# Kernel tuning notes

Hardware: AMD Instinct MI355X
Metric: run time of the kernel (lower is better)

## Reference

```python
import jax, jax.numpy as jnp
import numpy as np

B, S, H, NH = 4, 2048, 1024, 16
HD = H // NH


def setup_inputs() -> dict:
    key = jax.random.key(0)
    ks = jax.random.split(key, 8)
    x = jax.random.normal(ks[0], (B, S, H), dtype=jnp.float32)
    y = jax.random.normal(ks[1], (B, S, H), dtype=jnp.float32)
    mask = jnp.zeros((B, S), dtype=bool)  # key padding mask; True = masked
    s = 0.02
    Wq_w = jax.random.normal(ks[2], (H, H), dtype=jnp.float32) * s
    Wq_b = jnp.zeros((H,), dtype=jnp.float32)
    Wkv_w = jax.random.normal(ks[3], (H, 2 * H), dtype=jnp.float32) * s
    Wkv_b = jnp.zeros((2 * H,), dtype=jnp.float32)
    Wo_w = jax.random.normal(ks[4], (H, H), dtype=jnp.float32) * s
    Wo_b = jnp.zeros((H,), dtype=jnp.float32)
    return {"x": x, "y": y, "mask": mask, "Wq_w": Wq_w, "Wq_b": Wq_b,
            "Wkv_w": Wkv_w, "Wkv_b": Wkv_b, "Wo_w": Wo_w, "Wo_b": Wo_b}


def reference(x, y, mask, Wq_w, Wq_b, Wkv_w, Wkv_b, Wo_w, Wo_b):
    b, s, c = x.shape
    # q: [B, NH, S, HD]
    q = (x @ Wq_w + Wq_b).reshape(b, s, NH, HD).transpose(0, 2, 1, 3)
    # kv: [B, S, 2, NH, HD] -> k, v: [B, NH, S, HD]
    kv = (y @ Wkv_w + Wkv_b).reshape(b, s, 2, NH, HD)
    k = kv[:, :, 0].transpose(0, 2, 1, 3)
    v = kv[:, :, 1].transpose(0, 2, 1, 3)
    attn = jnp.einsum("bhqd,bhkd->bhqk", q, k) / jnp.sqrt(jnp.float32(HD))
    causal = jnp.triu(jnp.ones((s, s), dtype=bool), k=1)  # True above diag = masked
    combined = causal[None, None, :, :] | mask[:, None, None, :]
    attn = jnp.where(combined, -jnp.inf, attn)
    attn = jax.nn.softmax(attn, axis=-1)
    # dropout is identity in eval mode
    out = jnp.einsum("bhqk,bhkd->bhqd", attn, v)
    out = out.transpose(0, 2, 1, 3).reshape(b, s, c)
    return out @ Wo_w + Wo_b
```

## Files before the change

### kernel.cpp

```cpp
#include <hip/hip_runtime.h>


#define Bv   4
#define Sv   2048
#define Hv   1024
#define NHv  16
#define HDv  64

typedef __attribute__((ext_vector_type(8))) short s16x8;
typedef __attribute__((ext_vector_type(4))) short s16x4;
typedef __attribute__((ext_vector_type(4))) float f32x4;

__device__ __forceinline__ short f2bf(float f) {
  unsigned u = __float_as_uint(f);
  unsigned r = (u + 0x7fffu + ((u >> 16) & 1u)) >> 16;
  return (short)r;
}

#if __has_builtin(__builtin_amdgcn_exp2f)
#define EXP2(x) __builtin_amdgcn_exp2f(x)
#else
#define EXP2(x) exp2f(x)
#endif

__device__ __forceinline__ void gl_lds16(const short* g, short* l) {
  __builtin_amdgcn_global_load_lds(
      (const __attribute__((address_space(1))) unsigned int*)g,
      (__attribute__((address_space(3))) unsigned int*)l, 16, 0, 0);
}

__global__ __launch_bounds__(256) void cvt2_bf16(const float* __restrict__ x,
                                                 const float* __restrict__ y,
                                                 short* __restrict__ Xb,
                                                 short* __restrict__ Yb, int nper) {
  int half = gridDim.x >> 1;
  int bid = blockIdx.x;
  const float* in = (bid < half) ? x : y;
  short* out = (bid < half) ? Xb : Yb;
  int lb = (bid < half) ? bid : bid - half;
  int i = (lb * 256 + threadIdx.x) * 4;
  if (i < nper) {
    float4 v = *(const float4*)&in[i];
    short r0 = f2bf(v.x), r1 = f2bf(v.y), r2 = f2bf(v.z), r3 = f2bf(v.w);
    unsigned long long pk = (unsigned long long)(unsigned short)r0
                          | ((unsigned long long)(unsigned short)r1 << 16)
                          | ((unsigned long long)(unsigned short)r2 << 32)
                          | ((unsigned long long)(unsigned short)r3 << 48);
    *(unsigned long long*)&out[i] = pk;
  }
}

__global__ __launch_bounds__(256)
void tcvt3(const float* __restrict__ Wq, const float* __restrict__ Wkv,
           const float* __restrict__ Wo, short* __restrict__ Wt,
           short* __restrict__ Wot) {
  __shared__ float tile[32][33];
  int bx = blockIdx.x;
  const float* in;
  short* out;
  int C, cx;
  if (bx < 32)       { in = Wq;  out = Wt;                          C = 1024; cx = bx; }
  else if (bx < 96)  { in = Wkv; out = Wt + (size_t)Hv * Hv;        C = 2048; cx = bx - 32; }
  else               { in = Wo;  out = Wot;                         C = 1024; cx = bx - 96; }
  const int R = 1024;
  int tx = threadIdx.x & 31, ty = threadIdx.x >> 5;
  int c0 = cx * 32, r0 = blockIdx.y * 32;
#pragma unroll
  for (int i = 0; i < 32; i += 8)
    tile[ty + i][tx] = in[(size_t)(r0 + ty + i) * C + c0 + tx];
  __syncthreads();
#pragma unroll
  for (int i = 0; i < 32; i += 8)
    out[(size_t)(c0 + ty + i) * R + r0 + tx] = f2bf(tile[tx][ty + i]);
}

__global__ __launch_bounds__(256)
void gemm_qkv(const short* __restrict__ Xb, const short* __restrict__ Yb,
              const short* __restrict__ Wt, const float* __restrict__ Wqb,
              const float* __restrict__ Wkvb, short* __restrict__ Qb,
              short* __restrict__ Kb, short* __restrict__ Vt) {
  __shared__ union SMem {
    struct { short A[2][128 * 64]; short B[2][128 * 64]; } g;
    short ep[128 * 136];
  } sm;
  const int tid = threadIdx.x;
  const int w = tid >> 6, l = tid & 63;
  const int wr = w >> 1, wc = w & 1;
  const int m0 = blockIdx.x * 128, n0 = blockIdx.y * 128;
  const short* A = (n0 < 1024) ? Xb : Yb;
  const int sel = n0 >> 10;

  auto STAGE = [&](int k0, int bi) {
#pragma unroll
    for (int i = 0; i < 4; ++i) {
      int c = tid + i * 256;
      int r = c >> 3;
      int u = (c & 7) ^ (r & 7);
      gl_lds16(&A[(size_t)(m0 + r) * Hv + k0 + u * 8], &sm.g.A[bi][c * 8]);
      gl_lds16(&Wt[(size_t)(n0 + r) * Hv + k0 + u * 8], &sm.g.B[bi][c * 8]);
    }
  };

  f32x4 acc[4][4] = {};

  auto KSTEP = [&](int kt) {
    const int buf = kt & 1;
#pragma unroll
    for (int kk = 0; kk < 64; kk += 32) {
      s16x8 af[4], bf[4];
#pragma unroll
      for (int m = 0; m < 4; ++m) {
        int row = wr * 64 + m * 16 + (l & 15);
        int sb = (row * 128 + kk * 2 + ((l >> 4) << 4)) ^ ((row & 7) << 4);
        af[m] = *(s16x8*)((char*)sm.g.A[buf] + sb);
      }
#pragma unroll
      for (int n = 0; n < 4; ++n) {
        int row = wc * 64 + n * 16 + (l & 15);
        int sb = (row * 128 + kk * 2 + ((l >> 4) << 4)) ^ ((row & 7) << 4);
        bf[n] = *(s16x8*)((char*)sm.g.B[buf] + sb);
      }
#pragma unroll
      for (int m = 0; m < 4; ++m)
#pragma unroll
        for (int n = 0; n < 4; ++n)
          acc[m][n] = __builtin_amdgcn_mfma_f32_16x16x32_bf16(af[m], bf[n], acc[m][n], 0, 0, 0);
    }
  };

  STAGE(0, 0);
  STAGE(64, 1);

  for (int kt = 0; kt < 15; ++kt) {
    asm volatile("s_waitcnt vmcnt(8)" ::: "memory");
    __builtin_amdgcn_s_barrier();
    __builtin_amdgcn_sched_barrier(0);
    KSTEP(kt);
    __builtin_amdgcn_s_barrier();
    __builtin_amdgcn_sched_barrier(0);
    if (kt + 2 < 16) STAGE((kt + 2) * 64, kt & 1);
  }
  asm volatile("s_waitcnt vmcnt(0)" ::: "memory");
  __builtin_amdgcn_s_barrier();
  __builtin_amdgcn_sched_barrier(0);
  KSTEP(15);
  __syncthreads();

  const int b = m0 >> 11, s0 = m0 & (Sv - 1);
  if (sel < 2) {
    const float scale = (sel == 0) ? 0.1803368801f : 1.0f;
    const float* bias = (sel == 0) ? Wqb : (Wkvb + (n0 - 1024));
#pragma unroll
    for (int m = 0; m < 4; ++m)
#pragma unroll
      for (int n = 0; n < 4; ++n) {
        int scol = wc * 64 + n * 16 + (l & 15);
#pragma unroll
        for (int e = 0; e < 4; ++e) {
          int srow = wr * 64 + m * 16 + ((l >> 4) << 2) + e;
          float v = (acc[m][n][e] + bias[scol]) * scale;
          sm.ep[srow * 136 + scol] = f2bf(v);
        }
      }
    __syncthreads();
    short* dst = sel ? Kb : Qb;
    const int hbase = (n0 & 1023) >> 6;
#pragma unroll
    for (int p = 0; p < 8; ++p) {
      int u = p * 256 + tid;
      int row = u >> 4, hf = (u >> 3) & 1, sub = u & 7;
      s16x8 vdat = *(s16x8*)&sm.ep[row * 136 + hf * 64 + sub * 8];
      *(s16x8*)&dst[(((size_t)(b * NHv + hbase + hf)) * Sv + s0 + row) * HDv + sub * 8] = vdat;
    }
  } else {
    const float* bias = Wkvb + (n0 - 1024);
#pragma unroll
    for (int m = 0; m < 4; ++m)
#pragma unroll
      for (int n = 0; n < 4; ++n) {
        int scol = wc * 64 + n * 16 + (l & 15);
        int srow0 = wr * 64 + m * 16 + ((l >> 4) << 2);
        s16x4 t;
#pragma unroll
        for (int e = 0; e < 4; ++e) t[e] = f2bf(acc[m][n][e] + bias[scol]);
        *(s16x4*)&sm.ep[scol * 136 + srow0] = t;
      }
    __syncthreads();
    const int hbase = (n0 - 2048) >> 6;
#pragma unroll
    for (int p = 0; p < 8; ++p) {
      int u = p * 256 + tid;
      int col = u >> 4, seg = u & 15;
      s16x8 vdat = *(s16x8*)&sm.ep[col * 136 + seg * 8];
      *(s16x8*)&Vt[(((size_t)(b * NHv + hbase + (col >> 6))) * HDv + (col & 63)) * Sv + s0 + seg * 8] = vdat;
    }
  }
}

__global__ __launch_bounds__(256)
void gemm_out(const short* __restrict__ A, const short* __restrict__ Bt,
              const float* __restrict__ bias, float* __restrict__ outf) {
  __shared__ short Alds[2][128 * 64];
  __shared__ short Blds[2][128 * 64];
  const int tid = threadIdx.x;
  const int w = tid >> 6, l = tid & 63;
  const int wr = w >> 1, wc = w & 1;
  const int m0 = blockIdx.x * 128, n0 = blockIdx.y * 128;

  auto STAGE = [&](int k0, int bi) {
#pragma unroll
    for (int i = 0; i < 4; ++i) {
      int c = tid + i * 256;
      int r = c >> 3;
      int u = (c & 7) ^ (r & 7);
      gl_lds16(&A[(size_t)(m0 + r) * Hv + k0 + u * 8], &Alds[bi][c * 8]);
      gl_lds16(&Bt[(size_t)(n0 + r) * Hv + k0 + u * 8], &Blds[bi][c * 8]);
    }
  };

  f32x4 acc[4][4] = {};

  STAGE(0, 0);
  __syncthreads();
  for (int kt = 0; kt < 16; ++kt) {
    const int buf = kt & 1;
    if (kt < 15) STAGE((kt + 1) * 64, buf ^ 1);
#pragma unroll
    for (int kk = 0; kk < 64; kk += 32) {
      s16x8 af[4], bf[4];
#pragma unroll
      for (int m = 0; m < 4; ++m) {
        int row = wr * 64 + m * 16 + (l & 15);
        int sb = (row * 128 + kk * 2 + ((l >> 4) << 4)) ^ ((row & 7) << 4);
        af[m] = *(s16x8*)((char*)Alds[buf] + sb);
      }
#pragma unroll
      for (int n = 0; n < 4; ++n) {
        int row = wc * 64 + n * 16 + (l & 15);
        int sb = (row * 128 + kk * 2 + ((l >> 4) << 4)) ^ ((row & 7) << 4);
        bf[n] = *(s16x8*)((char*)Blds[buf] + sb);
      }
#pragma unroll
      for (int m = 0; m < 4; ++m)
#pragma unroll
        for (int n = 0; n < 4; ++n)
          acc[m][n] = __builtin_amdgcn_mfma_f32_16x16x32_bf16(af[m], bf[n], acc[m][n], 0, 0, 0);
    }
    __syncthreads();
  }

#pragma unroll
  for (int m = 0; m < 4; ++m)
#pragma unroll
    for (int n = 0; n < 4; ++n)
#pragma unroll
      for (int e = 0; e < 4; ++e) {
        int gr = m0 + wr * 64 + m * 16 + ((l >> 4) << 2) + e;
        int gc = n0 + wc * 64 + n * 16 + (l & 15);
        outf[(size_t)gr * Hv + gc] = acc[m][n][e] + bias[gc];
      }
}

__global__ __launch_bounds__(512)
void attn_mfma(const short* __restrict__ Q, const short* __restrict__ Kb,
               const short* __restrict__ Vt, const unsigned char* __restrict__ msk,
               short* __restrict__ AO) {
  __shared__ short Klds[2][64 * 64];
  __shared__ short Vlds[2][64 * 64];
  __shared__ short Plds[8 * 32 * 64];
  __shared__ unsigned long long mword[2];

  const int tid = threadIdx.x;
  const int w = tid >> 6, l = tid & 63;
  const int il = l & 15, g = l >> 4;
  const int bh = blockIdx.x & 63;
  const int qb = 7 - (blockIdx.x >> 6);
  const int b = bh >> 4, h = bh & 15;
  const int q0 = qb * 256 + w * 32;

  int kvA0[4], pfA0[2];
#pragma unroll
  for (int n = 0; n < 4; ++n) {
    int row = n * 16 + il;
    kvA0[n] = row * 128 + ((g << 4) ^ ((row & 7) << 4));
  }
#pragma unroll
  for (int m = 0; m < 2; ++m) {
    int row = m * 16 + il;
    pfA0[m] = row * 128 + ((g << 4) ^ ((row & 7) << 4));
  }
  const int swzq = (il & 7) << 4;
  const int g8 = g << 3;

  s16x8 qf[2][2];
  const short* qbase = &Q[((size_t)bh * Sv + q0) * HDv];
#pragma unroll
  for (int m = 0; m < 2; ++m)
#pragma unroll
    for (int kk = 0; kk < 2; ++kk)
      qf[m][kk] = *(const s16x8*)&qbase[(m * 16 + il) * 64 + kk * 32 + (g << 3)];

  s16x8 onesf;
#pragma unroll
  for (int e2 = 0; e2 < 8; ++e2) onesf[e2] = (short)0x3F80;

  f32x4 oacc[2][4] = {};
  f32x4 lacc[2] = {};
  const f32x4 cinit = {-16.f, -16.f, -16.f, -16.f};

  char* const pbase = (char*)Plds + w * 4096;
  const short* kg0 = &Kb[(size_t)bh * Sv * HDv];
  const short* vg0 = &Vt[(size_t)bh * HDv * Sv];
  const int nkt = qb * 4 + 4;

  auto stageKV = [&](int t, int bufi) {
    const short* kg = kg0 + (size_t)t * 64 * HDv;
    const short* vg = vg0 + t * 64;
    int c = tid;
    int r = c >> 3;
    int u = (c & 7) ^ (r & 7);
    gl_lds16(&kg[(size_t)r * HDv + u * 8], &Klds[bufi][c * 8]);
    gl_lds16(&vg[(size_t)r * Sv + u * 8], &Vlds[bufi][c * 8]);
  };

  stageKV(0, 0);
  if (w == 0) {
    unsigned long long mwb = __ballot(msk[b * Sv + l] != 0);
    if (l == 0) mword[0] = mwb;
  }
  __syncthreads();

  for (int kt = 0; kt < nkt; ++kt) {
    const int k0 = kt * 64;
    const int buf = kt & 1;
    if (kt + 1 < nkt) {
      stageKV(kt + 1, buf ^ 1);
      if (w == 0) {
        unsigned long long mwb = __ballot(msk[b * Sv + (kt + 1) * 64 + l] != 0);
        if (l == 0) mword[buf ^ 1] = mwb;
      }
    }

    if (k0 <= q0 + 31) {
      const unsigned long long mw = mword[buf];
      const char* kldsb = (const char*)Klds[buf];
      const char* vldsb = (const char*)Vlds[buf];
      f32x4 sacc[4][2];
#pragma unroll
      for (int n = 0; n < 4; ++n)
#pragma unroll
        for (int m = 0; m < 2; ++m)
          sacc[n][m] = cinit;
      __builtin_amdgcn_s_setprio(1);
#pragma unroll
      for (int kk = 0; kk < 2; ++kk) {
        s16x8 kf[4];
#pragma unroll
        for (int n = 0; n < 4; ++n)
          kf[n] = *(s16x8*)(kldsb + (kvA0[n] ^ (kk << 6)));
#pragma unroll
        for (int n = 0; n < 4; ++n)
#pragma unroll
          for (int m = 0; m < 2; ++m)
            sacc[n][m] = __builtin_amdgcn_mfma_f32_16x16x32_bf16(kf[n], qf[m][kk], sacc[n][m], 0, 0, 0);
      }
      __builtin_amdgcn_s_setprio(0);

      if ((k0 + 63 > q0) || (mw != 0)) {
#pragma unroll
        for (int n = 0; n < 4; ++n)
#pragma unroll
          for (int m = 0; m < 2; ++m)
#pragma unroll
            for (int e = 0; e < 4; ++e) {
              int klocal = n * 16 + (g << 2) + e;
              int qg = q0 + m * 16 + il;
              bool bad = (k0 + klocal > qg) || ((mw >> klocal) & 1ull);
              if (bad) sacc[n][m][e] = -1e30f;
            }
      }

#pragma unroll
      for (int kk = 0; kk < 2; ++kk) {
#pragma unroll
        for (int m = 0; m < 2; ++m) {
          int pwb = (m * 16 + il) * 128;
#pragma unroll
          for (int n = kk * 2; n < kk * 2 + 2; ++n) {
            s16x4 t;
#pragma unroll
            for (int e = 0; e < 4; ++e) {
              float pv = EXP2(sacc[n][m][e]);
              t[e] = (short)(__float_as_uint(pv) >> 16);
            }
            *(s16x4*)(pbase + pwb + (((n << 5) + g8) ^ swzq)) = t;
          }
        }
        s16x8 pf[2], vf[4];
#pragma unroll
        for (int m = 0; m < 2; ++m)
          pf[m] = *(s16x8*)(pbase + (pfA0[m] ^ (kk << 6)));
#pragma unroll
        for (int n = 0; n < 4; ++n)
          vf[n] = *(s16x8*)(vldsb + (kvA0[n] ^ (kk << 6)));
        __builtin_amdgcn_s_setprio(1);
#pragma unroll
        for (int m = 0; m < 2; ++m) {
#pragma unroll
          for (int n = 0; n < 4; ++n)
            oacc[m][n] = __builtin_amdgcn_mfma_f32_16x16x32_bf16(pf[m], vf[n], oacc[m][n], 0, 0, 0);
          lacc[m] = __builtin_amdgcn_mfma_f32_16x16x32_bf16(pf[m], onesf, lacc[m], 0, 0, 0);
        }
        __builtin_amdgcn_s_setprio(0);
      }
    }
    __syncthreads();
  }

#pragma unroll
  for (int m = 0; m < 2; ++m)
#pragma unroll
    for (int e = 0; e < 4; ++e) {
      float inv = 1.f / lacc[m][e];
#pragma unroll
      for (int n = 0; n < 4; ++n) {
        int qg = q0 + m * 16 + (g << 2) + e;
        int dcol = n * 16 + il;
        AO[((size_t)b * Sv + qg) * Hv + h * HDv + dcol] = f2bf(oacc[m][n][e] * inv);
      }
    }
}

extern "C" void kernel_launch(void* const* d_in, const int* in_sizes, int n_in,
                              void* d_out, int out_size, void* d_ws, size_t ws_size,
                              hipStream_t stream) {
  (void)in_sizes; (void)n_in; (void)out_size; (void)ws_size;
  const float* x    = (const float*)d_in[0];
  const float* y    = (const float*)d_in[1];
  const unsigned char* msk = (const unsigned char*)d_in[2];
  const float* Wq   = (const float*)d_in[3];
  const float* Wqb  = (const float*)d_in[4];
  const float* Wkv  = (const float*)d_in[5];
  const float* Wkvb = (const float*)d_in[6];
  const float* Wo   = (const float*)d_in[7];
  const float* Wob  = (const float*)d_in[8];
  float* out = (float*)d_out;

  char* p = (char*)d_ws;
  auto alloc = [&](size_t bytes) {
    char* r = p;
    p += (bytes + 255) & ~(size_t)255;
    return r;
  };
  const size_t MT = (size_t)Bv * Sv;
  short* Xb   = (short*)alloc(MT * Hv * 2);
  short* Yb   = (short*)alloc(MT * Hv * 2);
  short* Wt   = (short*)alloc((size_t)3 * Hv * Hv * 2);
  short* Wot  = (short*)alloc((size_t)Hv * Hv * 2);
  short* Qb   = (short*)alloc(MT * Hv * 2);
  short* Kb   = (short*)alloc(MT * Hv * 2);
  short* Vb   = (short*)alloc(MT * Hv * 2);
  short* AO   = (short*)alloc(MT * Hv * 2);

  const int n_x = (int)(MT * Hv);
  cvt2_bf16<<<2 * (n_x / 1024), 256, 0, stream>>>(x, y, Xb, Yb, n_x);
  tcvt3<<<dim3(128, 32), 256, 0, stream>>>(Wq, Wkv, Wo, Wt, Wot);

  gemm_qkv<<<dim3(64, 24), 256, 0, stream>>>(Xb, Yb, Wt, Wqb, Wkvb, Qb, Kb, Vb);

  attn_mfma<<<8 * 64, 512, 0, stream>>>(Qb, Kb, Vb, msk, AO);

  gemm_out<<<dim3(64, 8), 256, 0, stream>>>(AO, Wot, Wob, out);
}
```

Measured before the change: 157.9 us.

## Load K/V fragments directly from global memory instead of LDS staging

Removes the double-buffered LDS staging of K and V tiles and the block-wide barrier per key tile. Each wave now reads its K and V MFMA fragments straight from global memory (relying on L1/L2 caching), computes the mask ballot itself, and iterates only over the key tiles its own 32 queries need. This drops the synchronisation and LDS traffic, but every wave refetches the same K/V data from cache, with less latency hiding and smaller, strided V loads.

```diff
diff --git a/kernel.cpp b/kernel.cpp
--- a/kernel.cpp
+++ b/kernel.cpp
@@ -265,10 +265,7 @@
 void attn_mfma(const short* __restrict__ Q, const short* __restrict__ Kb,
                const short* __restrict__ Vt, const unsigned char* __restrict__ msk,
                short* __restrict__ AO) {
-  __shared__ short Klds[2][64 * 64];
-  __shared__ short Vlds[2][64 * 64];
   __shared__ short Plds[8 * 32 * 64];
-  __shared__ unsigned long long mword[2];
 
   const int tid = threadIdx.x;
   const int w = tid >> 6, l = tid & 63;
@@ -278,12 +275,7 @@
   const int b = bh >> 4, h = bh & 15;
   const int q0 = qb * 256 + w * 32;
 
-  int kvA0[4], pfA0[2];
-#pragma unroll
-  for (int n = 0; n < 4; ++n) {
-    int row = n * 16 + il;
-    kvA0[n] = row * 128 + ((g << 4) ^ ((row & 7) << 4));
-  }
+  int pfA0[2];
 #pragma unroll
   for (int m = 0; m < 2; ++m) {
     int row = m * 16 + il;
@@ -292,13 +284,23 @@
   const int swzq = (il & 7) << 4;
   const int g8 = g << 3;
 
+  const short* kg0 = &Kb[(size_t)bh * Sv * HDv];
+  const short* vg0 = &Vt[(size_t)bh * HDv * Sv];
+  const short* kfb[4];
+  const short* vfb[4];
+#pragma unroll
+  for (int n = 0; n < 4; ++n) {
+    kfb[n] = kg0 + (n * 16 + il) * 64 + g8;
+    vfb[n] = vg0 + (size_t)(n * 16 + il) * Sv + g8;
+  }
+
   s16x8 qf[2][2];
   const short* qbase = &Q[((size_t)bh * Sv + q0) * HDv];
 #pragma unroll
   for (int m = 0; m < 2; ++m)
 #pragma unroll
     for (int kk = 0; kk < 2; ++kk)
-      qf[m][kk] = *(const s16x8*)&qbase[(m * 16 + il) * 64 + kk * 32 + (g << 3)];
+      qf[m][kk] = *(const s16x8*)&qbase[(m * 16 + il) * 64 + kk * 32 + g8];
 
   s16x8 onesf;
 #pragma unroll
@@ -309,112 +311,84 @@
   const f32x4 cinit = {-16.f, -16.f, -16.f, -16.f};
 
   char* const pbase = (char*)Plds + w * 4096;
-  const short* kg0 = &Kb[(size_t)bh * Sv * HDv];
-  const short* vg0 = &Vt[(size_t)bh * HDv * Sv];
-  const int nkt = qb * 4 + 4;
-
-  auto stageKV = [&](int t, int bufi) {
-    const short* kg = kg0 + (size_t)t * 64 * HDv;
-    const short* vg = vg0 + t * 64;
-    int c = tid;
-    int r = c >> 3;
-    int u = (c & 7) ^ (r & 7);
-    gl_lds16(&kg[(size_t)r * HDv + u * 8], &Klds[bufi][c * 8]);
-    gl_lds16(&vg[(size_t)r * Sv + u * 8], &Vlds[bufi][c * 8]);
-  };
-
-  stageKV(0, 0);
-  if (w == 0) {
-    unsigned long long mwb = __ballot(msk[b * Sv + l] != 0);
-    if (l == 0) mword[0] = mwb;
-  }
-  __syncthreads();
+  const int nkt = (q0 >> 6) + 1;
+  const unsigned char* mrow = &msk[b * Sv + l];
 
   for (int kt = 0; kt < nkt; ++kt) {
     const int k0 = kt * 64;
-    const int buf = kt & 1;
-    if (kt + 1 < nkt) {
-      stageKV(kt + 1, buf ^ 1);
-      if (w == 0) {
-        unsigned long long mwb = __ballot(msk[b * Sv + (kt + 1) * 64 + l] != 0);
-        if (l == 0) mword[buf ^ 1] = mwb;
-      }
-    }
-
-    if (k0 <= q0 + 31) {
-      const unsigned long long mw = mword[buf];
-      const char* kldsb = (const char*)Klds[buf];
-      const char* vldsb = (const char*)Vlds[buf];
-      f32x4 sacc[4][2];
+    const unsigned long long mw = __ballot(mrow[k0] != 0);
+
+    f32x4 sacc[4][2];
+#pragma unroll
+    for (int n = 0; n < 4; ++n)
+#pragma unroll
+      for (int m = 0; m < 2; ++m)
+        sacc[n][m] = cinit;
+    {
+      s16x8 kf[4][2];
 #pragma unroll
       for (int n = 0; n < 4; ++n)
 #pragma unroll
+        for (int kk = 0; kk < 2; ++kk)
+          kf[n][kk] = *(const s16x8*)(kfb[n] + k0 * 64 + kk * 32);
+      __builtin_amdgcn_s_setprio(1);
+#pragma unroll
+      for (int kk = 0; kk < 2; ++kk)
+#pragma unroll
+        for (int n = 0; n < 4; ++n)
+#pragma unroll
+          for (int m = 0; m < 2; ++m)
+            sacc[n][m] = __builtin_amdgcn_mfma_f32_16x16x32_bf16(kf[n][kk], qf[m][kk], sacc[n][m], 0, 0, 0);
+      __builtin_amdgcn_s_setprio(0);
+    }
+
+    if ((k0 + 63 > q0) || (mw != 0)) {
+#pragma unroll
+      for (int n = 0; n < 4; ++n)
+#pragma unroll
         for (int m = 0; m < 2; ++m)
-          sacc[n][m] = cinit;
+#pragma unroll
+          for (int e = 0; e < 4; ++e) {
+            int klocal = n * 16 + (g << 2) + e;
+            int qg = q0 + m * 16 + il;
+            bool bad = (k0 + klocal > qg) || ((mw >> klocal) & 1ull);
+            if (bad) sacc[n][m][e] = -1e30f;
+          }
+    }
+
+#pragma unroll
+    for (int kk = 0; kk < 2; ++kk) {
+#pragma unroll
+      for (int m = 0; m < 2; ++m) {
+        int pwb = (m * 16 + il) * 128;
+#pragma unroll
+        for (int n = kk * 2; n < kk * 2 + 2; ++n) {
+          s16x4 t;
+#pragma unroll
+          for (int e = 0; e < 4; ++e) {
+            float pv = EXP2(sacc[n][m][e]);
+            t[e] = (short)(__float_as_uint(pv) >> 16);
+          }
+          *(s16x4*)(pbase + pwb + (((n << 5) + g8) ^ swzq)) = t;
+        }
+      }
+      s16x8 pf[2], vf[4];
+#pragma unroll
+      for (int m = 0; m < 2; ++m)
+        pf[m] = *(s16x8*)(pbase + (pfA0[m] ^ (kk << 6)));
+#pragma unroll
+      for (int n = 0; n < 4; ++n)
+        vf[n] = *(const s16x8*)(vfb[n] + k0 + kk * 32);
       __builtin_amdgcn_s_setprio(1);
 #pragma unroll
-      for (int kk = 0; kk < 2; ++kk) {
-        s16x8 kf[4];
+      for (int m = 0; m < 2; ++m) {
 #pragma unroll
         for (int n = 0; n < 4; ++n)
-          kf[n] = *(s16x8*)(kldsb + (kvA0[n] ^ (kk << 6)));
-#pragma unroll
-        for (int n = 0; n < 4; ++n)
-#pragma unroll
-          for (int m = 0; m < 2; ++m)
-            sacc[n][m] = __builtin_amdgcn_mfma_f32_16x16x32_bf16(kf[n], qf[m][kk], sacc[n][m], 0, 0, 0);
+          oacc[m][n] = __builtin_amdgcn_mfma_f32_16x16x32_bf16(pf[m], vf[n], oacc[m][n], 0, 0, 0);
+        lacc[m] = __builtin_amdgcn_mfma_f32_16x16x32_bf16(pf[m], onesf, lacc[m], 0, 0, 0);
       }
       __builtin_amdgcn_s_setprio(0);
-
-      if ((k0 + 63 > q0) || (mw != 0)) {
-#pragma unroll
-        for (int n = 0; n < 4; ++n)
-#pragma unroll
-          for (int m = 0; m < 2; ++m)
-#pragma unroll
-            for (int e = 0; e < 4; ++e) {
-              int klocal = n * 16 + (g << 2) + e;
-              int qg = q0 + m * 16 + il;
-              bool bad = (k0 + klocal > qg) || ((mw >> klocal) & 1ull);
-              if (bad) sacc[n][m][e] = -1e30f;
-            }
-      }
-
-#pragma unroll
-      for (int kk = 0; kk < 2; ++kk) {
-#pragma unroll
-        for (int m = 0; m < 2; ++m) {
-          int pwb = (m * 16 + il) * 128;
-#pragma unroll
-          for (int n = kk * 2; n < kk * 2 + 2; ++n) {
-            s16x4 t;
-#pragma unroll
-            for (int e = 0; e < 4; ++e) {
-              float pv = EXP2(sacc[n][m][e]);
-              t[e] = (short)(__float_as_uint(pv) >> 16);
-            }
-            *(s16x4*)(pbase + pwb + (((n << 5) + g8) ^ swzq)) = t;
-          }
-        }
-        s16x8 pf[2], vf[4];
-#pragma unroll
-        for (int m = 0; m < 2; ++m)
-          pf[m] = *(s16x8*)(pbase + (pfA0[m] ^ (kk << 6)));
-#pragma unroll
-        for (int n = 0; n < 4; ++n)
-          vf[n] = *(s16x8*)(vldsb + (kvA0[n] ^ (kk << 6)));
-        __builtin_amdgcn_s_setprio(1);
-#pragma unroll
-        for (int m = 0; m < 2; ++m) {
-#pragma unroll
-          for (int n = 0; n < 4; ++n)
-            oacc[m][n] = __builtin_amdgcn_mfma_f32_16x16x32_bf16(pf[m], vf[n], oacc[m][n], 0, 0, 0);
-          lacc[m] = __builtin_amdgcn_mfma_f32_16x16x32_bf16(pf[m], onesf, lacc[m], 0, 0, 0);
-        }
-        __builtin_amdgcn_s_setprio(0);
-      }
-    }
-    __syncthreads();
+    }
   }
 
 #pragma unroll
```

Measured after the change: 225.9 us. 1.43x slower.
